# Kernel optimization log

Measured on AMD Instinct MI355X. Metric: run time of the kernel, lower is better.

Reference implementation:

```python
import jax, jax.numpy as jnp
import numpy as np
import math

# static config (see shape_source)
NUM_GRAPHS = 8      # b
L_NODES = 1024      # nodes per graph (uniform -> to_dense_batch is a reshape)
D_INNER = 128
HEADDIM = 16
N_HEADS = D_INNER // HEADDIM  # 8
D_STATE = 64
NUM_DT = 4          # 3 node-dt components + dt_self
AVG_DEG = 16
DIAMETER = 50       # default_graph_diameter
TOL = 0.1
DT_MIN, DT_MAX, DT_FLOOR = 1e-3, 1e-1, 1e-4


def dag_inverse(A):
    """DAGInverse.forward: (I - A)^{-1} via repeated-squaring doubling.
    A: [b, h, l, l]. j = 2^ceil(log2(diameter)); out = prod (I + A^{2^k})."""
    j = 2 ** math.ceil(math.log2(DIAMETER))  # 64
    I = jnp.eye(A.shape[-1], dtype=A.dtype)
    last = A
    out = I + A
    for _ in range(2, int(math.log2(j)) + 1):  # 5 iterations
        last = last @ last
        out = out @ (I + last)
    return out


def setup_inputs() -> dict:
    key = jax.random.key(0)
    k = jax.random.split(key, 8)
    N = NUM_GRAPHS * L_NODES
    x = jax.random.normal(k[0], (N, D_INNER), jnp.float32)
    B_mat = jax.random.normal(k[1], (N, D_STATE), jnp.float32)
    C_mat = jax.random.normal(k[2], (N, D_STATE), jnp.float32)
    dt = jax.random.normal(k[3], (N, NUM_DT * N_HEADS), jnp.float32)
    # dt_bias init as in GraphSSD.__init__
    u = jax.random.uniform(k[4], (N_HEADS,), jnp.float32)
    dt0 = jnp.exp(u * (math.log(DT_MAX) - math.log(DT_MIN)) + math.log(DT_MIN))
    dt0 = jnp.clip(dt0, DT_FLOOR, None)
    dt_bias = dt0 + jnp.log(-jnp.expm1(-dt0))
    D = jnp.ones((N_HEADS,), jnp.float32)
    # edges: per-graph random endpoints, offset to global node ids
    E_per = L_NODES * AVG_DEG
    src_l = jax.random.randint(k[5], (NUM_GRAPHS, E_per), 0, L_NODES)
    dst_l = jax.random.randint(k[6], (NUM_GRAPHS, E_per), 0, L_NODES)
    off = (jnp.arange(NUM_GRAPHS) * L_NODES)[:, None]
    edge_index = jnp.stack([(src_l + off).reshape(-1), (dst_l + off).reshape(-1)], 0).astype(jnp.int32)
    return {"x": x, "B_mat": B_mat, "C_mat": C_mat, "dt": dt,
            "dt_bias": dt_bias, "D": D, "edge_index": edge_index}


def reference(x, B_mat, C_mat, dt, dt_bias, D, edge_index):
    Bn, Lg, H, hd, ds = NUM_GRAPHS, L_NODES, N_HEADS, HEADDIM, D_STATE
    N = Bn * Lg
    # dense batching (uniform graph sizes -> pure reshape, mask all True)
    x_d = x.reshape(Bn, Lg, H, hd).transpose(0, 2, 1, 3)        # b n l h ('(n h)' split)
    B_d = B_mat.reshape(Bn, Lg, ds)                             # broadcast over heads
    C_d = C_mat.reshape(Bn, Lg, ds)
    # dt: 'l (n c) -> c n l'
    dt_c = dt.reshape(N, H, NUM_DT).transpose(2, 1, 0)          # c n l
    dt_node, dt_self = dt_c[:NUM_DT - 1], dt_c[NUM_DT - 1]      # (3,n,N), (n,N)
    dt_self_d = dt_self.T.reshape(Bn, Lg, H).transpose(0, 2, 1)  # b n l
    # multiply_dt_w_A: A = -exp(A_log)= -1 (with_A=False)
    dt_A_node = -jax.nn.softplus(dt_node + dt_bias[None, :, None])  # (3, n, N)
    # edge dt: (dt_s[src] + dt_t[dst]) / 2, then exp
    src, dst = edge_index[0], edge_index[1]
    attr = jnp.exp((dt_A_node[0][:, src] + dt_A_node[1][:, dst]) * 0.5).T  # (E, n)
    # to_dense_adj scatter: [b, l1, l2, h] then -> b h l1 l2
    b_idx, sl, dl = src // Lg, src % Lg, dst % Lg
    A_mat = jnp.zeros((Bn, Lg, Lg, H), x.dtype).at[b_idx, sl, dl].add(attr)
    A_mat = A_mat.transpose(0, 3, 1, 2)                          # b n l1 l2
    # 'leq' normalization with dummy self term
    dt_dummy = jnp.exp(dt_A_node[2]).T.reshape(Bn, Lg, H).transpose(0, 2, 1)  # b n l
    normalizer = A_mat.sum(-1) + dt_dummy                        # b n l1
    A_norm = A_mat / (normalizer[..., None] + TOL)
    # L = (I - A^T)^{-1} via DAGInverse doubling
    Lmat = dag_inverse(jnp.swapaxes(A_norm, -1, -2).astype(jnp.float32))  # b n l t
    L_norm = Lmat * dt_self_d[:, :, None, :]                     # scale along t
    # y = einsum(C, L, B, x); C/B broadcast in heads -> G shared across heads
    G = jnp.einsum('bld,btd->blt', C_d, B_d)[:, None]            # b 1 l t
    y = jnp.einsum('bnlt,bnth->bnlh', L_norm * G, x_d)
    y = y + x_d * D[None, :, None, None]
    # 'b n l h -> b l (h n)'
    y = y.transpose(0, 2, 3, 1).reshape(Bn, Lg, H * hd)
    return y.reshape(N, H * hd)
```

## Files before the change

kernel.cpp:

```cpp
#include <hip/hip_runtime.h>
#include <hip/hip_bf16.h>

#define H_ 8
#define NTOT 8192
#define LG 1024
#define BN 8
#define HD 16
#define DSTATE 64
#define EPG 16384
#define MSZ (1024*1024)

typedef __hip_bfloat16 bf16;
typedef unsigned short ushort_t;
typedef _Float16 f16;
typedef __attribute__((ext_vector_type(8))) _Float16 half8;
typedef __attribute__((ext_vector_type(4))) _Float16 half4;
typedef __attribute__((ext_vector_type(4))) float f4v;

__device__ __forceinline__ float b2f(bf16 v){ return __bfloat162float(v); }
__device__ __forceinline__ float sp_(float z){
  return fmaxf(z, 0.f) + log1pf(expf(-fabsf(z)));
}
__device__ __forceinline__ float ldv(const void* p, size_t i, int f32){
  float v;
  if (f32) v = ((const float*)p)[i];
  else     v = b2f(((const bf16*)p)[i]);
  return v;
}
__device__ __forceinline__ void gl2lds16(const void* g, void* l){
  __builtin_amdgcn_global_load_lds((const __attribute__((address_space(1))) unsigned int*)g,
                                   (__attribute__((address_space(3))) unsigned int*)l,
                                   16, 0, 0);
}

__global__ void k_sniff(const void* __restrict__ dt, int* __restrict__ flag){
  const ushort_t* p = (const ushort_t*)dt;
  int tid = threadIdx.x;
  int bad = 0;
  for (int i = tid; i < 512; i += 256){
    int e = (p[i] >> 7) & 0xFF;
    if (e >= 140) bad = 1;
  }
  unsigned long long m = __ballot(bad != 0);
  __shared__ int anybad[4];
  if ((tid & 63) == 0) anybad[tid >> 6] = (m != 0ull) ? 1 : 0;
  __syncthreads();
  if (tid == 0) *flag = (anybad[0] | anybad[1] | anybad[2] | anybad[3]);
}

__global__ void k_nodecoef(const void* __restrict__ dt, const void* __restrict__ dtb,
                           const int* __restrict__ flag,
                           float* __restrict__ a0, float* __restrict__ a1,
                           float* __restrict__ dum, float* __restrict__ sdt){
  int idx = blockIdx.x*256 + threadIdx.x;
  if (idx >= H_*NTOT) return;
  int f32 = *flag;
  int h = idx / NTOT, n = idx - h*NTOT;
  float bias = ldv(dtb, h, f32);
  size_t base = (size_t)n*(4*H_) + h*4;
  float d0, d1, d2, d3;
  if (f32){
    const float* row = (const float*)dt + base;
    d0 = row[0]; d1 = row[1]; d2 = row[2]; d3 = row[3];
  } else {
    const bf16* row = (const bf16*)dt + base;
    d0 = b2f(row[0]); d1 = b2f(row[1]); d2 = b2f(row[2]); d3 = b2f(row[3]);
  }
  a0[(size_t)n*H_ + h] = -sp_(d0 + bias);
  a1[(size_t)n*H_ + h] = -sp_(d1 + bias);
  dum[idx] = expf(-sp_(d2 + bias));
  sdt[idx] = d3;
}

__global__ __launch_bounds__(256) void k_zero(char* base, size_t regB, float* __restrict__ nrm){
  int bh = blockIdx.y;
  if (blockIdx.x < 1024){
    float* Mf = (float*)(base + (size_t)bh*regB) + MSZ;
    int i = blockIdx.x*1024 + threadIdx.x*4;
    *(float4*)(Mf + i) = make_float4(0.f,0.f,0.f,0.f);
  } else {
    int j = threadIdx.x*4;
    *(float4*)(nrm + (size_t)bh*LG + j) = make_float4(0.f,0.f,0.f,0.f);
  }
}

__global__ void k_scatter(const int* __restrict__ ei, const float* __restrict__ a0,
                          const float* __restrict__ a1, char* base, size_t regB,
                          float* __restrict__ nrm,
                          int b0, int h0, int lgHB, int GBp, int nthreads, int Etot){
  int t = blockIdx.x*256 + threadIdx.x;
  if (t >= nthreads) return;
  int HB = 1 << lgHB;
  int hl = t & (HB-1);
  int el = t >> lgHB;
  int e = b0*EPG + el;
  int src = ei[e], dst = ei[Etot + e];
  int g = src >> 10;
  if ((unsigned)(g - b0) >= (unsigned)GBp) return;
  int sl = src & 1023, dl = dst & 1023;
  int h = h0 + hl;
  float attr = expf(0.5f*(a0[(size_t)src*H_ + h] + a1[(size_t)dst*H_ + h]));
  int bhl = (g - b0)*HB + hl;
  float* Mf = (float*)(base + (size_t)bhl*regB) + MSZ;
  atomicAdd(&Mf[(size_t)dl*LG + sl], attr);
  atomicAdd(&nrm[bhl*LG + sl], attr);
}

__global__ __launch_bounds__(256) void k_norm2(char* base, size_t regB,
                            const float* __restrict__ nrm, const float* __restrict__ dum,
                            int b0, int h0, int HB){
  __shared__ ushort_t tb[32][33];
  int bh = blockIdx.z;
  int g = b0 + bh / HB, h = h0 + bh % HB;
  const float* Mf = (const float*)(base + (size_t)bh*regB) + MSZ;
  f16* L0  = (f16*)(base + (size_t)bh*regB);
  f16* L0T = L0 + MSZ;
  f16* O0  = L0 + (size_t)4*MSZ;
  int x0 = blockIdx.x*32, y0 = blockIdx.y*32;
  int tx = threadIdx.x & 31, ty = threadIdx.x >> 5;
  int sl = x0 + tx;
  float denom = nrm[(size_t)bh*LG + sl] + dum[(size_t)h*NTOT + g*LG + sl] + 0.1f;
  float rden = 1.f / denom;
  #pragma unroll
  for (int i = 0; i < 32; i += 8){
    int dl = y0 + ty + i;
    float v = Mf[(size_t)dl*LG + sl] * rden;
    f16 hv = (f16)v;
    L0[(size_t)dl*LG + sl] = hv;
    O0[(size_t)dl*LG + sl] = (f16)(v + (dl == sl ? 1.f : 0.f));
    union { f16 h; ushort_t u; } cv; cv.h = hv;
    tb[tx][ty + i] = cv.u;
  }
  __syncthreads();
  #pragma unroll
  for (int i = 0; i < 32; i += 8){
    union { f16 h; ushort_t u; } cv; cv.u = tb[ty + i][tx];
    L0T[(size_t)(x0 + ty + i)*LG + y0 + tx] = cv.h;
  }
}

__global__ __launch_bounds__(256) void k_G(const void* __restrict__ Bm, const void* __restrict__ Cm,
                                           const int* __restrict__ flag,
                                           f16* __restrict__ G, int b0){
  int gl = blockIdx.z;
  int g = b0 + gl;
  int l0 = blockIdx.y*16, t0 = blockIdx.x*16;
  __shared__ float Cs[16][DSTATE+1];
  __shared__ float Bs[16][DSTATE+1];
  int tid = threadIdx.x;
  int f32 = *flag;
  if (f32){
    const float* Cf = (const float*)Cm;
    const float* Bf = (const float*)Bm;
    for (int i = tid; i < 16*DSTATE; i += 256){
      int r = i >> 6, d = i & 63;
      Cs[r][d] = Cf[(size_t)(g*LG + l0 + r)*DSTATE + d];
      Bs[r][d] = Bf[(size_t)(g*LG + t0 + r)*DSTATE + d];
    }
  } else {
    const bf16* Cb = (const bf16*)Cm;
    const bf16* Bb = (const bf16*)Bm;
    for (int i = tid; i < 16*DSTATE; i += 256){
      int r = i >> 6, d = i & 63;
      Cs[r][d] = b2f(Cb[(size_t)(g*LG + l0 + r)*DSTATE + d]);
      Bs[r][d] = b2f(Bb[(size_t)(g*LG + t0 + r)*DSTATE + d]);
    }
  }
  __syncthreads();
  int r = tid >> 4, c = tid & 15;
  float acc = 0.f;
  #pragma unroll
  for (int d = 0; d < DSTATE; ++d) acc = fmaf(Cs[r][d], Bs[c][d], acc);
  G[(size_t)gl*MSZ + (size_t)(l0+r)*LG + t0 + c] = (f16)acc;
}

__global__ __launch_bounds__(512, 6) void k_gemm_fused(char* base, size_t regB,
    int nS, int iAs, int iBTs, int iCs, int iCTs,
    int nU, int iAu, int iBTu, int iCu){
  __shared__ ushort_t As[2][4096];
  __shared__ ushort_t Bs[2][4096];
  int T = nS + nU;
  int s = blockIdx.x + 8*blockIdx.z;
  if (s >= T) return;
  int isS = (s < nS) ? 1 : 0;
  int bh  = isS ? s : (s - nS);
  int iA  = isS ? iAs : iAu;
  int iBT = isS ? iBTs : iBTu;
  int iC  = isS ? iCs : iCu;
  int iCT = isS ? iCTs : -1;
  int addA = 1 - isS;
  char* reg = base + (size_t)bh*regB;
  const f16* Ab = (const f16*)reg + (size_t)iA*MSZ;
  const f16* Bb = (const f16*)reg + (size_t)iBT*MSZ;
  f16* Cb = (f16*)reg + (size_t)iC*MSZ;
  int y = blockIdx.y;
  int i0 = (y >> 3)*128, j0 = (y & 7)*128;
  int tid = threadIdx.x;
  int lane = tid & 63, wv = tid >> 6;
  int wr = (wv >> 2)*64, wc = (wv & 3)*32;
  int m16 = lane & 15, q = lane >> 4;
  int srow = tid >> 2;
  int skq = (tid & 3) ^ ((tid >> 3) & 3);
  const f16* Ag = Ab + (size_t)(i0 + srow)*LG + skq*8;
  const f16* Bg = Bb + (size_t)(j0 + srow)*LG + skq*8;
  #define STAGE(K0, BUF) do { \
    gl2lds16(Ag + (K0), &As[BUF][(size_t)tid*8]); \
    gl2lds16(Bg + (K0), &Bs[BUF][(size_t)tid*8]); } while(0)
  STAGE(0, 0);
  f4v acc[4][2] = {};
  int slotq = q ^ ((m16 >> 1) & 3);
  int aoff = (wr + m16)*32 + slotq*8;
  int boff = (wc + m16)*32 + slotq*8;
  for (int k0 = 0; k0 < LG; k0 += 32){
    int cur = (k0 >> 5) & 1;
    __syncthreads();
    if (k0 + 32 < LG) STAGE(k0 + 32, cur ^ 1);
    half8 af[4], bfr[2];
    #pragma unroll
    for (int t = 0; t < 4; ++t)
      af[t]  = *(const half8*)&As[cur][aoff + t*512];
    #pragma unroll
    for (int t = 0; t < 2; ++t)
      bfr[t] = *(const half8*)&Bs[cur][boff + t*512];
    #pragma unroll
    for (int mt = 0; mt < 4; ++mt)
      #pragma unroll
      for (int nt = 0; nt < 2; ++nt)
        acc[mt][nt] = __builtin_amdgcn_mfma_f32_16x16x32_f16(af[mt], bfr[nt], acc[mt][nt], 0, 0, 0);
  }
  #undef STAGE
  f16* CT = (f16*)reg + (size_t)((iCT < 0) ? iC : iCT)*MSZ;
  #pragma unroll
  for (int mt = 0; mt < 4; ++mt){
    #pragma unroll
    for (int nt = 0; nt < 2; ++nt){
      int gr0 = i0 + wr + mt*16 + q*4;
      int gc = j0 + wc + nt*16 + m16;
      half4 tv;
      #pragma unroll
      for (int r = 0; r < 4; ++r){
        float v = acc[mt][nt][r];
        if (addA) v += (float)Ab[(size_t)(gr0 + r)*LG + gc];
        f16 hv = (f16)v;
        tv[r] = hv;
        Cb[(size_t)(gr0 + r)*LG + gc] = hv;
      }
      if (iCT >= 0)
        *(half4*)&CT[(size_t)gc*LG + gr0] = tv;
    }
  }
}

__global__ __launch_bounds__(256) void k_final2(char* base, size_t regB, int iO,
    const f16* __restrict__ Gh, const float* __restrict__ sdt,
    const void* __restrict__ x, const void* __restrict__ Dv,
    const int* __restrict__ flag, void* __restrict__ out,
    int b0, int h0, int HB){
  __shared__ float coef[16][257];
  int bh = blockIdx.y;
  int gl = bh / HB, g = b0 + gl, h = h0 + bh % HB;
  int L0r = blockIdx.x*16;
  int tid = threadIdx.x;
  int lr = tid >> 4, ts = tid & 15;
  int f32 = *flag;
  const f16* Orow = (const f16*)(base + (size_t)bh*regB) + (size_t)iO*MSZ + (size_t)(L0r+lr)*LG;
  const f16* Grow = Gh + (size_t)gl*MSZ + (size_t)(L0r+lr)*LG;
  const float* srow = sdt + (size_t)h*NTOT + g*LG;
  float acc = 0.f;
  for (int tc = 0; tc < LG; tc += 256){
    int tb = tc + ts*16;
    __syncthreads();
    half8 o0 = *(const half8*)&Orow[tb];
    half8 o1 = *(const half8*)&Orow[tb + 8];
    half8 g0 = *(const half8*)&Grow[tb];
    half8 g1 = *(const half8*)&Grow[tb + 8];
    #pragma unroll
    for (int j = 0; j < 8; ++j){
      coef[lr][ts*16 + j]     = (float)o0[j] * (float)g0[j] * srow[tb + j];
      coef[lr][ts*16 + 8 + j] = (float)o1[j] * (float)g1[j] * srow[tb + 8 + j];
    }
    __syncthreads();
    if (f32){
      const float* xf = (const float*)x + (size_t)(g*LG + tc)*128 + h*HD + ts;
      for (int t = 0; t < 256; ++t)
        acc = fmaf(coef[lr][t], xf[(size_t)t*128], acc);
    } else {
      const bf16* xb = (const bf16*)x + (size_t)(g*LG + tc)*128 + h*HD + ts;
      for (int t = 0; t < 256; ++t)
        acc = fmaf(coef[lr][t], b2f(xb[(size_t)t*128]), acc);
    }
  }
  int l = L0r + lr, d = ts;
  float xs = ldv(x, (size_t)(g*LG + l)*128 + h*HD + d, f32);
  float dv = ldv(Dv, h, f32);
  float v = acc + xs*dv;
  size_t off = (size_t)(g*LG + l)*128 + d*H_ + h;
  if (f32) ((float*)out)[off] = v;
  else     ((bf16*)out)[off] = __float2bfloat16(v);
}

extern "C" void kernel_launch(void* const* d_in, const int* in_sizes, int n_in,
                              void* d_out, int out_size, void* d_ws, size_t ws_size,
                              hipStream_t stream){
  const void* x   = d_in[0];
  const void* Bm  = d_in[1];
  const void* Cm  = d_in[2];
  const void* dt  = d_in[3];
  const void* dtb = d_in[4];
  const void* Dv  = d_in[5];
  const int*  ei  = (const int*)d_in[6];
  int Etot = in_sizes[6] / 2;

  const size_t REG = (size_t)6*MSZ*2;
  int GB = 1, HB = 1;
  const int cfgs[7][2] = {{8,8},{4,8},{2,8},{1,8},{1,4},{1,2},{1,1}};
  for (int i = 0; i < 7; ++i){
    int gb = cfgs[i][0], hb = cfgs[i][1];
    size_t need = 4ull*(4ull*H_*NTOT + 64)
                + 4ull*(size_t)gb*hb*LG
                + 2ull*(size_t)gb*MSZ
                + (size_t)gb*hb*REG;
    if (need <= ws_size){ GB = gb; HB = hb; break; }
  }
  int lgHB = (HB==8)?3:((HB==4)?2:((HB==2)?1:0));
  int nbh = GB*HB;

  float* a0  = (float*)d_ws;
  float* a1  = a0 + H_*NTOT;
  float* dum = a1 + H_*NTOT;
  float* sdt = dum + H_*NTOT;
  int*  flag = (int*)(sdt + H_*NTOT);
  float* nrm = (float*)flag + 64;
  f16* G     = (f16*)(nrm + (size_t)nbh*LG);
  char* chainBase = (char*)(G + (size_t)GB*MSZ);

  k_sniff<<<1, 256, 0, stream>>>(dt, flag);
  k_nodecoef<<<(H_*NTOT + 255)/256, 256, 0, stream>>>(dt, dtb, flag, a0, a1, dum, sdt);

  for (int b0 = 0; b0 < BN; b0 += GB){
    for (int h0 = 0; h0 < H_; h0 += HB){
      k_zero<<<dim3(1025, nbh), 256, 0, stream>>>(chainBase, REG, nrm);
      int nthr = GB*EPG*HB;
      k_scatter<<<(nthr + 255)/256, 256, 0, stream>>>(ei, a0, a1, chainBase, REG, nrm,
                                                      b0, h0, lgHB, GB, nthr, Etot);
      k_norm2<<<dim3(32, 32, nbh), 256, 0, stream>>>(chainBase, REG, nrm, dum, b0, h0, HB);
      if (h0 == 0){
        dim3 gg(64, 64, GB);
        k_G<<<gg, 256, 0, stream>>>(Bm, Cm, flag, G, b0);
      }
      int lA = 0, lAT = 1, lC = 2, lCT = 3, oA = 4, oC = 5;
      {
        int T = nbh;
        dim3 gg(8, 64, (T + 7)/8);
        k_gemm_fused<<<gg, 512, 0, stream>>>(chainBase, REG, nbh, lA, lAT, lC, lCT,
                                             0, 0, 0, 0);
      }
      for (int k = 0; k < 4; ++k){
        int T = 2*nbh;
        dim3 gg(8, 64, (T + 7)/8);
        k_gemm_fused<<<gg, 512, 0, stream>>>(chainBase, REG,
                                             nbh, lC, lCT, lA, lAT,
                                             nbh, oA, lCT, oC);
        int tp;
        tp = lA; lA = lC; lC = tp;
        tp = lAT; lAT = lCT; lCT = tp;
        tp = oA; oA = oC; oC = tp;
      }
      {
        int T = nbh;
        dim3 gg(8, 64, (T + 7)/8);
        k_gemm_fused<<<gg, 512, 0, stream>>>(chainBase, REG, 0, 0, 0, 0, 0,
                                             nbh, oA, lCT, oC);
        int tp = oA; oA = oC; oC = tp;
      }
      dim3 fg(64, nbh);
      k_final2<<<fg, 256, 0, stream>>>(chainBase, REG, oA, G, sdt, x, Dv, flag, d_out, b0, h0, HB);
    }
  }
}
```

Before: 2.449 ms.

## Rewrite fused GEMM with 256x256 tiles and deep global-to-LDS pipeline

Replaces the 128x128 tile GEMM with a 256x256 output tile per block that uses 128KB of dynamic LDS. The new kernel has a multi-stage global_load_lds prefetch ring with explicit vmcnt waits, split barriers, s_setprio around the MFMA bursts, and a new XOR swizzle. The goal is more operand reuse per loaded byte and better overlap of loads with MFMA work in the dense 1024x1024 chain products. In exchange, occupancy drops to about one block per CU and there are far fewer blocks per launch (16 per matrix), which risks poor CU fill when nbh is small.

```diff
diff --git a/kernel.cpp b/kernel.cpp
--- a/kernel.cpp
+++ b/kernel.cpp
@@ -32,6 +32,8 @@
                                    (__attribute__((address_space(3))) unsigned int*)l,
                                    16, 0, 0);
 }
+
+#define BARC() do { asm volatile("" ::: "memory"); __builtin_amdgcn_s_barrier(); asm volatile("" ::: "memory"); } while(0)
 
 __global__ void k_sniff(const void* __restrict__ dt, int* __restrict__ flag){
   const ushort_t* p = (const ushort_t*)dt;
@@ -174,13 +176,12 @@
   G[(size_t)gl*MSZ + (size_t)(l0+r)*LG + t0 + c] = (f16)acc;
 }
 
-__global__ __launch_bounds__(512, 6) void k_gemm_fused(char* base, size_t regB,
+__global__ __launch_bounds__(512, 2) void k_gemm_fused(char* base, size_t regB,
     int nS, int iAs, int iBTs, int iCs, int iCTs,
     int nU, int iAu, int iBTu, int iCu){
-  __shared__ ushort_t As[2][4096];
-  __shared__ ushort_t Bs[2][4096];
+  extern __shared__ char lds[];
   int T = nS + nU;
-  int s = blockIdx.x + 8*blockIdx.z;
+  int s = blockIdx.z;
   if (s >= T) return;
   int isS = (s < nS) ? 1 : 0;
   int bh  = isS ? s : (s - nS);
@@ -193,49 +194,106 @@
   const f16* Ab = (const f16*)reg + (size_t)iA*MSZ;
   const f16* Bb = (const f16*)reg + (size_t)iBT*MSZ;
   f16* Cb = (f16*)reg + (size_t)iC*MSZ;
-  int y = blockIdx.y;
-  int i0 = (y >> 3)*128, j0 = (y & 7)*128;
+  int i0 = blockIdx.y*256, j0 = blockIdx.x*256;
   int tid = threadIdx.x;
   int lane = tid & 63, wv = tid >> 6;
-  int wr = (wv >> 2)*64, wc = (wv & 3)*32;
+  int wm = wv >> 2, wn = wv & 3;
   int m16 = lane & 15, q = lane >> 4;
-  int srow = tid >> 2;
-  int skq = (tid & 3) ^ ((tid >> 3) & 3);
-  const f16* Ag = Ab + (size_t)(i0 + srow)*LG + skq*8;
-  const f16* Bg = Bb + (size_t)(j0 + srow)*LG + skq*8;
-  #define STAGE(K0, BUF) do { \
-    gl2lds16(Ag + (K0), &As[BUF][(size_t)tid*8]); \
-    gl2lds16(Bg + (K0), &Bs[BUF][(size_t)tid*8]); } while(0)
-  STAGE(0, 0);
-  f4v acc[4][2] = {};
-  int slotq = q ^ ((m16 >> 1) & 3);
-  int aoff = (wr + m16)*32 + slotq*8;
-  int boff = (wc + m16)*32 + slotq*8;
-  for (int k0 = 0; k0 < LG; k0 += 32){
-    int cur = (k0 >> 5) & 1;
-    __syncthreads();
-    if (k0 + 32 < LG) STAGE(k0 + 32, cur ^ 1);
-    half8 af[4], bfr[2];
-    #pragma unroll
-    for (int t = 0; t < 4; ++t)
-      af[t]  = *(const half8*)&As[cur][aoff + t*512];
-    #pragma unroll
-    for (int t = 0; t < 2; ++t)
-      bfr[t] = *(const half8*)&Bs[cur][boff + t*512];
+  int rswz  = m16*128 + ((q ^ (m16 & 7)) << 4);
+  int rswz1 = rswz ^ 64;
+  int bcol = (wn & 1) << 13;
+  int sr = tid >> 3;
+  int sc = (tid & 7) ^ (sr & 7);
+
+  auto ISSUE = [&](int h){
+    if (h >= 64) return;
+    int j = h & 3;
+    const f16* M = (j < 2) ? Bb : Ab;
+    int rb = ((j < 2) ? j0 : i0) + ((j & 1) << 7);
+    const f16* src = M + (size_t)(rb + sr)*LG + ((h >> 2) << 6) + sc*8;
+    char* dst = lds + ((h & 7) << 14) + tid*16;
+    gl2lds16(src, dst);
+    gl2lds16(src + (size_t)64*LG, dst + 8192);
+  };
+
+  ISSUE(0); ISSUE(1); ISSUE(2); ISSUE(3); ISSUE(4); ISSUE(5);
+  f4v acc[8][4] = {};
+  half8 af[4], bfr[2][4];
+  asm volatile("s_waitcnt vmcnt(4)" ::: "memory");
+  BARC();
+
+  for (int kt = 0; kt < 16; ++kt){
+    int sb = (kt & 1) << 2;
+    const char* Asl = lds + ((sb + 2 + wm) << 14);
+    const char* Bsl = lds + ((sb + (wn >> 1)) << 14) + bcol;
+    int h0 = kt*4 + 6;
+    #pragma unroll
+    for (int t = 0; t < 4; ++t) af[t] = *(const half8*)(Asl + t*2048 + rswz);
+    #pragma unroll
+    for (int t = 0; t < 4; ++t) bfr[0][t] = *(const half8*)(Bsl + t*2048 + rswz);
+    ISSUE(h0);
+    BARC();
+    asm volatile("s_waitcnt lgkmcnt(0)" ::: "memory");
+    __builtin_amdgcn_s_setprio(1);
     #pragma unroll
     for (int mt = 0; mt < 4; ++mt)
       #pragma unroll
-      for (int nt = 0; nt < 2; ++nt)
-        acc[mt][nt] = __builtin_amdgcn_mfma_f32_16x16x32_f16(af[mt], bfr[nt], acc[mt][nt], 0, 0, 0);
-  }
-  #undef STAGE
+      for (int nt = 0; nt < 4; ++nt)
+        acc[mt][nt] = __builtin_amdgcn_mfma_f32_16x16x32_f16(af[mt], bfr[0][nt], acc[mt][nt], 0, 0, 0);
+    __builtin_amdgcn_s_setprio(0);
+    BARC();
+    #pragma unroll
+    for (int t = 0; t < 4; ++t) af[t] = *(const half8*)(Asl + 8192 + t*2048 + rswz);
+    #pragma unroll
+    for (int t = 0; t < 4; ++t) bfr[1][t] = *(const half8*)(Bsl + t*2048 + rswz1);
+    ISSUE(h0 + 1);
+    BARC();
+    asm volatile("s_waitcnt lgkmcnt(0)" ::: "memory");
+    __builtin_amdgcn_s_setprio(1);
+    #pragma unroll
+    for (int mt = 0; mt < 4; ++mt)
+      #pragma unroll
+      for (int nt = 0; nt < 4; ++nt)
+        acc[4 + mt][nt] = __builtin_amdgcn_mfma_f32_16x16x32_f16(af[mt], bfr[0][nt], acc[4 + mt][nt], 0, 0, 0);
+    __builtin_amdgcn_s_setprio(0);
+    BARC();
+    #pragma unroll
+    for (int t = 0; t < 4; ++t) af[t] = *(const half8*)(Asl + t*2048 + rswz1);
+    ISSUE(h0 + 2);
+    BARC();
+    asm volatile("s_waitcnt lgkmcnt(0)" ::: "memory");
+    __builtin_amdgcn_s_setprio(1);
+    #pragma unroll
+    for (int mt = 0; mt < 4; ++mt)
+      #pragma unroll
+      for (int nt = 0; nt < 4; ++nt)
+        acc[mt][nt] = __builtin_amdgcn_mfma_f32_16x16x32_f16(af[mt], bfr[1][nt], acc[mt][nt], 0, 0, 0);
+    __builtin_amdgcn_s_setprio(0);
+    BARC();
+    #pragma unroll
+    for (int t = 0; t < 4; ++t) af[t] = *(const half8*)(Asl + 8192 + t*2048 + rswz1);
+    ISSUE(h0 + 3);
+    BARC();
+    asm volatile("s_waitcnt lgkmcnt(0)" ::: "memory");
+    __builtin_amdgcn_s_setprio(1);
+    #pragma unroll
+    for (int mt = 0; mt < 4; ++mt)
+      #pragma unroll
+      for (int nt = 0; nt < 4; ++nt)
+        acc[4 + mt][nt] = __builtin_amdgcn_mfma_f32_16x16x32_f16(af[mt], bfr[1][nt], acc[4 + mt][nt], 0, 0, 0);
+    __builtin_amdgcn_s_setprio(0);
+    if (kt < 14)       asm volatile("s_waitcnt vmcnt(4)" ::: "memory");
+    else if (kt == 14) asm volatile("s_waitcnt vmcnt(0)" ::: "memory");
+    BARC();
+  }
+
   f16* CT = (f16*)reg + (size_t)((iCT < 0) ? iC : iCT)*MSZ;
   #pragma unroll
-  for (int mt = 0; mt < 4; ++mt){
-    #pragma unroll
-    for (int nt = 0; nt < 2; ++nt){
-      int gr0 = i0 + wr + mt*16 + q*4;
-      int gc = j0 + wc + nt*16 + m16;
+  for (int mt = 0; mt < 8; ++mt){
+    #pragma unroll
+    for (int nt = 0; nt < 4; ++nt){
+      int gr0 = i0 + wm*128 + mt*16 + q*4;
+      int gc  = j0 + wn*64 + nt*16 + m16;
       half4 tv;
       #pragma unroll
       for (int r = 0; r < 4; ++r){
@@ -311,6 +369,13 @@
   const int*  ei  = (const int*)d_in[6];
   int Etot = in_sizes[6] / 2;
 
+  static int attrDone = 0;
+  if (!attrDone){
+    hipFuncSetAttribute(reinterpret_cast<const void*>(k_gemm_fused),
+                        hipFuncAttributeMaxDynamicSharedMemorySize, 131072);
+    attrDone = 1;
+  }
+
   const size_t REG = (size_t)6*MSZ*2;
   int GB = 1, HB = 1;
   const int cfgs[7][2] = {{8,8},{4,8},{2,8},{1,8},{1,4},{1,2},{1,1}};
@@ -350,27 +415,24 @@
       }
       int lA = 0, lAT = 1, lC = 2, lCT = 3, oA = 4, oC = 5;
       {
-        int T = nbh;
-        dim3 gg(8, 64, (T + 7)/8);
-        k_gemm_fused<<<gg, 512, 0, stream>>>(chainBase, REG, nbh, lA, lAT, lC, lCT,
-                                             0, 0, 0, 0);
+        dim3 gg(4, 4, nbh);
+        k_gemm_fused<<<gg, 512, 131072, stream>>>(chainBase, REG, nbh, lA, lAT, lC, lCT,
+                                                  0, 0, 0, 0);
       }
       for (int k = 0; k < 4; ++k){
-        int T = 2*nbh;
-        dim3 gg(8, 64, (T + 7)/8);
-        k_gemm_fused<<<gg, 512, 0, stream>>>(chainBase, REG,
-                                             nbh, lC, lCT, lA, lAT,
-                                             nbh, oA, lCT, oC);
+        dim3 gg(4, 4, 2*nbh);
+        k_gemm_fused<<<gg, 512, 131072, stream>>>(chainBase, REG,
+                                                  nbh, lC, lCT, lA, lAT,
+                                                  nbh, oA, lCT, oC);
         int tp;
         tp = lA; lA = lC; lC = tp;
         tp = lAT; lAT = lCT; lCT = tp;
         tp = oA; oA = oC; oC = tp;
       }
       {
-        int T = nbh;
-        dim3 gg(8, 64, (T + 7)/8);
-        k_gemm_fused<<<gg, 512, 0, stream>>>(chainBase, REG, 0, 0, 0, 0, 0,
-                                             nbh, oA, lCT, oC);
+        dim3 gg(4, 4, nbh);
+        k_gemm_fused<<<gg, 512, 131072, stream>>>(chainBase, REG, 0, 0, 0, 0, 0,
+                                                  nbh, oA, lCT, oC);
         int tp = oA; oA = oC; oC = tp;
       }
       dim3 fg(64, nbh);
```

New measurement: 2.671 ms. 1.09x slower.

## Enlarge GEMM tile to 256x256 with four-stage LDS pipeline and 1024 threads

Applied to the files above, without the earlier changes.

Rewrites the fp16 MFMA GEMM in the doubling chain to use 256x256 output tiles per 1024-thread block, staging A and B through a four-deep dynamic-LDS ring of 128 KB. Loads are issued asynchronously with explicit vmcnt waits and raw barriers, and MFMA priority is raised. The aim is more operand reuse per LDS load, fewer global reads and better latency hiding. In exchange, occupancy per CU drops and the grid becomes much smaller, which risks underfilling the GPU when the batch is small.

```diff
diff --git a/kernel.cpp b/kernel.cpp
--- a/kernel.cpp
+++ b/kernel.cpp
@@ -32,6 +32,8 @@
                                    (__attribute__((address_space(3))) unsigned int*)l,
                                    16, 0, 0);
 }
+
+#define BARC() do { asm volatile("" ::: "memory"); __builtin_amdgcn_s_barrier(); asm volatile("" ::: "memory"); } while(0)
 
 __global__ void k_sniff(const void* __restrict__ dt, int* __restrict__ flag){
   const ushort_t* p = (const ushort_t*)dt;
@@ -174,11 +176,10 @@
   G[(size_t)gl*MSZ + (size_t)(l0+r)*LG + t0 + c] = (f16)acc;
 }
 
-__global__ __launch_bounds__(512, 6) void k_gemm_fused(char* base, size_t regB,
+__global__ __launch_bounds__(1024, 4) void k_gemm_fused(char* base, size_t regB,
     int nS, int iAs, int iBTs, int iCs, int iCTs,
     int nU, int iAu, int iBTu, int iCu){
-  __shared__ ushort_t As[2][4096];
-  __shared__ ushort_t Bs[2][4096];
+  extern __shared__ char lds[];
   int T = nS + nU;
   int s = blockIdx.x + 8*blockIdx.z;
   if (s >= T) return;
@@ -194,48 +195,69 @@
   const f16* Bb = (const f16*)reg + (size_t)iBT*MSZ;
   f16* Cb = (f16*)reg + (size_t)iC*MSZ;
   int y = blockIdx.y;
-  int i0 = (y >> 3)*128, j0 = (y & 7)*128;
+  int i0 = (y >> 2)*256, j0 = (y & 3)*256;
   int tid = threadIdx.x;
   int lane = tid & 63, wv = tid >> 6;
-  int wr = (wv >> 2)*64, wc = (wv & 3)*32;
+  int wm = wv >> 2, wn = wv & 3;
   int m16 = lane & 15, q = lane >> 4;
-  int srow = tid >> 2;
-  int skq = (tid & 3) ^ ((tid >> 3) & 3);
-  const f16* Ag = Ab + (size_t)(i0 + srow)*LG + skq*8;
-  const f16* Bg = Bb + (size_t)(j0 + srow)*LG + skq*8;
-  #define STAGE(K0, BUF) do { \
-    gl2lds16(Ag + (K0), &As[BUF][(size_t)tid*8]); \
-    gl2lds16(Bg + (K0), &Bs[BUF][(size_t)tid*8]); } while(0)
-  STAGE(0, 0);
-  f4v acc[4][2] = {};
-  int slotq = q ^ ((m16 >> 1) & 3);
-  int aoff = (wr + m16)*32 + slotq*8;
-  int boff = (wc + m16)*32 + slotq*8;
-  for (int k0 = 0; k0 < LG; k0 += 32){
-    int cur = (k0 >> 5) & 1;
-    __syncthreads();
-    if (k0 + 32 < LG) STAGE(k0 + 32, cur ^ 1);
-    half8 af[4], bfr[2];
+  int swz = (q ^ ((m16 >> 1) & 3)) << 4;
+  int aoff = (((wm & 1) << 6) + m16)*64 + swz;
+  int boff = (((wn & 1) << 6) + m16)*64 + swz;
+  int tl = tid & 511;
+  int sr = tl >> 2;
+  int sc = (tl & 3) ^ ((sr >> 1) & 3);
+
+  auto ISSUE2 = [&](int hA){
+    if (hA >= 128) return;
+    int h = (tid < 512) ? hA : (hA + 1);
+    int j = h & 3;
+    int kt2 = h >> 2;
+    const f16* M = (j < 2) ? Ab : Bb;
+    int rb = ((j < 2) ? i0 : j0) + ((j & 1) << 7);
+    const f16* src = M + (size_t)(rb + sr)*LG + kt2*32 + sc*8;
+    char* dst = lds + ((h & 15) << 13) + tl*16;
+    gl2lds16(src, dst);
+  };
+
+  ISSUE2(0); ISSUE2(2);
+  ISSUE2(4); ISSUE2(6);
+  ISSUE2(8); ISSUE2(10);
+  f4v acc[4][4] = {};
+  half8 af[4], bfr[4];
+  asm volatile("s_waitcnt vmcnt(4)" ::: "memory");
+  BARC();
+
+  for (int kt = 0; kt < 32; ++kt){
+    int sb = (kt & 3) << 2;
+    const char* Asl = lds + ((sb + (wm >> 1)) << 13);
+    const char* Bsl = lds + ((sb + 2 + (wn >> 1)) << 13);
     #pragma unroll
-    for (int t = 0; t < 4; ++t)
-      af[t]  = *(const half8*)&As[cur][aoff + t*512];
+    for (int t = 0; t < 4; ++t) af[t]  = *(const half8*)(Asl + aoff + t*1024);
     #pragma unroll
-    for (int t = 0; t < 2; ++t)
-      bfr[t] = *(const half8*)&Bs[cur][boff + t*512];
+    for (int t = 0; t < 4; ++t) bfr[t] = *(const half8*)(Bsl + boff + t*1024);
+    int hn = 4*(kt + 3);
+    ISSUE2(hn); ISSUE2(hn + 2);
+    asm volatile("s_waitcnt lgkmcnt(0)" ::: "memory");
+    __builtin_amdgcn_s_setprio(1);
     #pragma unroll
     for (int mt = 0; mt < 4; ++mt)
       #pragma unroll
-      for (int nt = 0; nt < 2; ++nt)
+      for (int nt = 0; nt < 4; ++nt)
         acc[mt][nt] = __builtin_amdgcn_mfma_f32_16x16x32_f16(af[mt], bfr[nt], acc[mt][nt], 0, 0, 0);
-  }
-  #undef STAGE
+    __builtin_amdgcn_s_setprio(0);
+    if (kt <= 28)      asm volatile("s_waitcnt vmcnt(4)" ::: "memory");
+    else if (kt == 29) asm volatile("s_waitcnt vmcnt(2)" ::: "memory");
+    else if (kt == 30) asm volatile("s_waitcnt vmcnt(0)" ::: "memory");
+    BARC();
+  }
+
   f16* CT = (f16*)reg + (size_t)((iCT < 0) ? iC : iCT)*MSZ;
   #pragma unroll
   for (int mt = 0; mt < 4; ++mt){
     #pragma unroll
-    for (int nt = 0; nt < 2; ++nt){
-      int gr0 = i0 + wr + mt*16 + q*4;
-      int gc = j0 + wc + nt*16 + m16;
+    for (int nt = 0; nt < 4; ++nt){
+      int gr0 = i0 + wm*64 + mt*16 + q*4;
+      int gc  = j0 + wn*64 + nt*16 + m16;
       half4 tv;
       #pragma unroll
       for (int r = 0; r < 4; ++r){
@@ -311,6 +333,13 @@
   const int*  ei  = (const int*)d_in[6];
   int Etot = in_sizes[6] / 2;
 
+  static int attrDone = 0;
+  if (!attrDone){
+    hipFuncSetAttribute(reinterpret_cast<const void*>(k_gemm_fused),
+                        hipFuncAttributeMaxDynamicSharedMemorySize, 131072);
+    attrDone = 1;
+  }
+
   const size_t REG = (size_t)6*MSZ*2;
   int GB = 1, HB = 1;
   const int cfgs[7][2] = {{8,8},{4,8},{2,8},{1,8},{1,4},{1,2},{1,1}};
@@ -351,16 +380,16 @@
       int lA = 0, lAT = 1, lC = 2, lCT = 3, oA = 4, oC = 5;
       {
         int T = nbh;
-        dim3 gg(8, 64, (T + 7)/8);
-        k_gemm_fused<<<gg, 512, 0, stream>>>(chainBase, REG, nbh, lA, lAT, lC, lCT,
-                                             0, 0, 0, 0);
+        dim3 gg(8, 16, (T + 7)/8);
+        k_gemm_fused<<<gg, 1024, 131072, stream>>>(chainBase, REG, nbh, lA, lAT, lC, lCT,
+                                                   0, 0, 0, 0);
       }
       for (int k = 0; k < 4; ++k){
         int T = 2*nbh;
-        dim3 gg(8, 64, (T + 7)/8);
-        k_gemm_fused<<<gg, 512, 0, stream>>>(chainBase, REG,
-                                             nbh, lC, lCT, lA, lAT,
-                                             nbh, oA, lCT, oC);
+        dim3 gg(8, 16, (T + 7)/8);
+        k_gemm_fused<<<gg, 1024, 131072, stream>>>(chainBase, REG,
+                                                   nbh, lC, lCT, lA, lAT,
+                                                   nbh, oA, lCT, oC);
         int tp;
         tp = lA; lA = lC; lC = tp;
         tp = lAT; lAT = lCT; lCT = tp;
@@ -368,9 +397,9 @@
       }
       {
         int T = nbh;
-        dim3 gg(8, 64, (T + 7)/8);
-        k_gemm_fused<<<gg, 512, 0, stream>>>(chainBase, REG, 0, 0, 0, 0, 0,
-                                             nbh, oA, lCT, oC);
+        dim3 gg(8, 16, (T + 7)/8);
+        k_gemm_fused<<<gg, 1024, 131072, stream>>>(chainBase, REG, 0, 0, 0, 0, 0,
+                                                   nbh, oA, lCT, oC);
         int tp = oA; oA = oC; oC = tp;
       }
       dim3 fg(64, nbh);
```

After: 2.258 ms (median of 2 runs). 7.8% less time.
